# Optimization experiments

Measured on AMD Instinct MI355X. Metric: run time of the kernel, lower is better.

The kernel has to match this reference:

```python
import jax, jax.numpy as jnp
import numpy as np

B, E, S = 32, 1024, 1024


def setup_inputs() -> dict:
    key = jax.random.key(0)
    k_x, k_w = jax.random.split(key)
    x = jax.random.normal(k_x, (B, E, S), dtype=jnp.float32)
    weight = jax.random.normal(k_w, (1, S), dtype=jnp.float32)
    bias = jnp.zeros((S,), dtype=jnp.float32)
    return {"x": x, "weight": weight, "bias": bias}


def _toeplitz(v):
    # v: (m,) -> M[i, j] = v[j - i] if j >= i else 0  (upper-triangular Toeplitz)
    m = v.shape[0]
    i = jnp.arange(m)[:, None]
    j = jnp.arange(m)[None, :]
    return jnp.where(j >= i, v[(j - i) % m], jnp.zeros((), dtype=v.dtype))


def reference(x, weight, bias):
    b, e, s = x.shape
    W = _toeplitz(weight.reshape(-1))          # (S, S)
    out = x.reshape(b * e, s) @ W + bias       # (B*E, S)
    return out.reshape(b, e, s)
```

## Files before the change

kernel.cpp:

```cpp
#include <hip/hip_runtime.h>
#include <stdint.h>

typedef __bf16 bf16x8 __attribute__((ext_vector_type(8)));
typedef float  f32x4  __attribute__((ext_vector_type(4)));

static constexpr int S_DIM = 1024;

__device__ __forceinline__ ushort f32_to_bf16_rne(float f) {
    uint32_t u = __builtin_bit_cast(uint32_t, f);
    u += 0x7fffu + ((u >> 16) & 1u);
    return (ushort)(u >> 16);
}
__device__ __forceinline__ uint32_t pk_bf16(float a, float b) {
    return (uint32_t)f32_to_bf16_rne(a) | ((uint32_t)f32_to_bf16_rne(b) << 16);
}

__global__ void build_wc(const float* __restrict__ w, ushort* __restrict__ Wc) {
    int c  = blockIdx.x * 256 + threadIdx.x;
    int kq = c >> 10;
    int j  = c & 1023;
    uint32_t p[4];
#pragma unroll
    for (int h = 0; h < 4; ++h) {
        int d0 = j - (kq * 8 + h * 2);
        int d1 = d0 - 1;
        float v0 = (d0 >= 0) ? w[d0] : 0.0f;
        float v1 = (d1 >= 0) ? w[d1] : 0.0f;
        p[h] = (uint32_t)f32_to_bf16_rne(v0) | ((uint32_t)f32_to_bf16_rne(v1) << 16);
    }
    reinterpret_cast<uint4*>(Wc)[c] = make_uint4(p[0], p[1], p[2], p[3]);
}

__global__ __launch_bounds__(512, 2) void toep_rowpanel64(
    const float* __restrict__ x, const ushort* __restrict__ Wc,
    const float* __restrict__ bias, float* __restrict__ out)
{
    __shared__ __align__(16) ushort As[2][2048];

    const int tid  = threadIdx.x;
    const int lane = tid & 63;
    const int w    = tid >> 6;
    const int l15  = lane & 15;
    const int quad = lane >> 4;
    const int m0   = blockIdx.x * 64;

    const int sm = tid >> 3;
    const int kc = tid & 7;
    const float* gx = x + (size_t)(m0 + sm) * S_DIM + kc * 4;
    const int aw = (kc >> 1) * 512 + sm * 8 + (kc & 1) * 4;

    const ushort* gb = Wc + (size_t)quad * 8192 + w * 256 + l15 * 8;

    const int ar0 = quad * 512 + l15 * 8;

    f32x4 acc[4][2][4] = {};

    f32x4 av0 = __builtin_nontemporal_load(reinterpret_cast<const f32x4*>(gx));
    f32x4 av1 = __builtin_nontemporal_load(reinterpret_cast<const f32x4*>(gx + 32));

    for (int it = 0; it < 32; ++it) {
        const int p = it & 1;

        uint32_t c0 = pk_bf16(av0[0], av0[1]);
        uint32_t c1 = pk_bf16(av0[2], av0[3]);
        *reinterpret_cast<uint2*>(&As[p][aw]) = make_uint2(c0, c1);

        bool g[4];
#pragma unroll
        for (int pi = 0; pi < 4; ++pi) g[pi] = (pi * 8 + w) >= it;

        const ushort* gbit = gb + (size_t)it * 32768;
        bf16x8 bf[4][2];
        if (g[0]) {
            bf[0][0] = *reinterpret_cast<const bf16x8*>(gbit + 0 * 2048);
            bf[0][1] = *reinterpret_cast<const bf16x8*>(gbit + 0 * 2048 + 128);
        }
        if (g[1]) {
            bf[1][0] = *reinterpret_cast<const bf16x8*>(gbit + 1 * 2048);
            bf[1][1] = *reinterpret_cast<const bf16x8*>(gbit + 1 * 2048 + 128);
        }
        if (g[2]) {
            bf[2][0] = *reinterpret_cast<const bf16x8*>(gbit + 2 * 2048);
            bf[2][1] = *reinterpret_cast<const bf16x8*>(gbit + 2 * 2048 + 128);
        }
        if (g[3]) {
            bf[3][0] = *reinterpret_cast<const bf16x8*>(gbit + 3 * 2048);
            bf[3][1] = *reinterpret_cast<const bf16x8*>(gbit + 3 * 2048 + 128);
        }

        int itn = it + 2; if (itn > 31) itn = 31;
        f32x4 avn = __builtin_nontemporal_load(reinterpret_cast<const f32x4*>(gx + itn * 32));

        asm volatile("s_waitcnt lgkmcnt(0)" ::: "memory");
        __builtin_amdgcn_s_barrier();
        asm volatile("" ::: "memory");

        bf16x8 af[4];
#pragma unroll
        for (int im = 0; im < 4; ++im)
            af[im] = *reinterpret_cast<const bf16x8*>(&As[p][ar0 + im * 128]);

        if (g[0]) {
#pragma unroll
            for (int h = 0; h < 2; ++h)
#pragma unroll
                for (int im = 0; im < 4; ++im)
                    acc[0][h][im] = __builtin_amdgcn_mfma_f32_16x16x32_bf16(af[im], bf[0][h], acc[0][h][im], 0, 0, 0);
        }
        if (g[1]) {
#pragma unroll
            for (int h = 0; h < 2; ++h)
#pragma unroll
                for (int im = 0; im < 4; ++im)
                    acc[1][h][im] = __builtin_amdgcn_mfma_f32_16x16x32_bf16(af[im], bf[1][h], acc[1][h][im], 0, 0, 0);
        }
        if (g[2]) {
#pragma unroll
            for (int h = 0; h < 2; ++h)
#pragma unroll
                for (int im = 0; im < 4; ++im)
                    acc[2][h][im] = __builtin_amdgcn_mfma_f32_16x16x32_bf16(af[im], bf[2][h], acc[2][h][im], 0, 0, 0);
        }
        if (g[3]) {
#pragma unroll
            for (int h = 0; h < 2; ++h)
#pragma unroll
                for (int im = 0; im < 4; ++im)
                    acc[3][h][im] = __builtin_amdgcn_mfma_f32_16x16x32_bf16(af[im], bf[3][h], acc[3][h][im], 0, 0, 0);
        }

        av0 = av1; av1 = avn;
    }

#pragma unroll
    for (int pi = 0; pi < 4; ++pi) {
        const int colb = pi * 256 + w * 32 + l15;
        const float bv0 = bias[colb];
        const float bv1 = bias[colb + 16];
#pragma unroll
        for (int im = 0; im < 4; ++im) {
            const int row0 = m0 + im * 16 + quad * 4;
            float* op = out + (size_t)row0 * S_DIM + colb;
#pragma unroll
            for (int r = 0; r < 4; ++r) {
                __builtin_nontemporal_store(acc[pi][0][im][r] + bv0, op + (size_t)r * S_DIM);
                __builtin_nontemporal_store(acc[pi][1][im][r] + bv1, op + (size_t)r * S_DIM + 16);
            }
        }
    }
}

extern "C" void kernel_launch(void* const* d_in, const int* in_sizes, int n_in,
                              void* d_out, int out_size, void* d_ws, size_t ws_size,
                              hipStream_t stream) {
    const float* x      = (const float*)d_in[0];
    const float* weight = (const float*)d_in[1];
    const float* bias   = (const float*)d_in[2];
    float* out          = (float*)d_out;

    ushort* Wc = (ushort*)d_ws;

    build_wc<<<512, 256, 0, stream>>>(weight, Wc);
    toep_rowpanel64<<<512, 512, 0, stream>>>(x, Wc, bias, out);
}
```

Measured before the change: 271.6 us.

## Stage A panel in 8-step phases to cut barriers per K iteration

The main loop is regrouped into 4 phases of 8 K-steps. Each phase stages a 64x256 bf16 slab of x in a double-buffered LDS array and prefetches the next slab's eight global loads at the start of the phase. This replaces a block barrier every K-step with one barrier per phase, and lets warps skip masked-out steps without synchronising. The cost is larger LDS use (64 KB) and more live registers for the prefetched vectors, which may hurt occupancy at 2 blocks per CU.

```diff
diff --git a/kernel.cpp b/kernel.cpp
--- a/kernel.cpp
+++ b/kernel.cpp
@@ -31,11 +31,11 @@
     reinterpret_cast<uint4*>(Wc)[c] = make_uint4(p[0], p[1], p[2], p[3]);
 }
 
-__global__ __launch_bounds__(512, 2) void toep_rowpanel64(
+__global__ __launch_bounds__(512, 2) void toep_phase64(
     const float* __restrict__ x, const ushort* __restrict__ Wc,
     const float* __restrict__ bias, float* __restrict__ out)
 {
-    __shared__ __align__(16) ushort As[2][2048];
+    __shared__ __align__(16) ushort As[2][8][2048];
 
     const int tid  = threadIdx.x;
     const int lane = tid & 63;
@@ -55,81 +55,101 @@
 
     f32x4 acc[4][2][4] = {};
 
-    f32x4 av0 = __builtin_nontemporal_load(reinterpret_cast<const f32x4*>(gx));
-    f32x4 av1 = __builtin_nontemporal_load(reinterpret_cast<const f32x4*>(gx + 32));
+    {
+        f32x4 v0[8];
+#pragma unroll
+        for (int kk = 0; kk < 8; ++kk)
+            v0[kk] = __builtin_nontemporal_load(reinterpret_cast<const f32x4*>(gx + kk * 32));
+#pragma unroll
+        for (int kk = 0; kk < 8; ++kk)
+            *reinterpret_cast<uint2*>(&As[0][kk][aw]) =
+                make_uint2(pk_bf16(v0[kk][0], v0[kk][1]), pk_bf16(v0[kk][2], v0[kk][3]));
+    }
+    __syncthreads();
 
-    for (int it = 0; it < 32; ++it) {
-        const int p = it & 1;
+    for (int p = 0; p < 4; ++p) {
+        const int b = p & 1;
+        f32x4 v[8];
 
-        uint32_t c0 = pk_bf16(av0[0], av0[1]);
-        uint32_t c1 = pk_bf16(av0[2], av0[3]);
-        *reinterpret_cast<uint2*>(&As[p][aw]) = make_uint2(c0, c1);
+#pragma unroll
+        for (int kk = 0; kk < 8; ++kk) {
+            const int it = p * 8 + kk;
+            const bool g0 = (w      ) >= it;
+            const bool g1 = (w +  8 ) >= it;
+            const bool g2 = (w + 16 ) >= it;
+            const bool g3 = (w + 24 ) >= it;
+            if (!g3) continue;
 
-        bool g[4];
+            const ushort* gbit = gb + (size_t)it * 32768;
+            bf16x8 bf[4][2];
+            if (g0) {
+                bf[0][0] = *reinterpret_cast<const bf16x8*>(gbit);
+                bf[0][1] = *reinterpret_cast<const bf16x8*>(gbit + 128);
+            }
+            if (g1) {
+                bf[1][0] = *reinterpret_cast<const bf16x8*>(gbit + 2048);
+                bf[1][1] = *reinterpret_cast<const bf16x8*>(gbit + 2048 + 128);
+            }
+            if (g2) {
+                bf[2][0] = *reinterpret_cast<const bf16x8*>(gbit + 4096);
+                bf[2][1] = *reinterpret_cast<const bf16x8*>(gbit + 4096 + 128);
+            }
+            if (g3) {
+                bf[3][0] = *reinterpret_cast<const bf16x8*>(gbit + 6144);
+                bf[3][1] = *reinterpret_cast<const bf16x8*>(gbit + 6144 + 128);
+            }
+
+            if (kk == 0 && p < 3) {
+                const float* gxn = gx + (p + 1) * 256;
 #pragma unroll
-        for (int pi = 0; pi < 4; ++pi) g[pi] = (pi * 8 + w) >= it;
+                for (int j = 0; j < 8; ++j)
+                    v[j] = __builtin_nontemporal_load(reinterpret_cast<const f32x4*>(gxn + j * 32));
+            }
 
-        const ushort* gbit = gb + (size_t)it * 32768;
-        bf16x8 bf[4][2];
-        if (g[0]) {
-            bf[0][0] = *reinterpret_cast<const bf16x8*>(gbit + 0 * 2048);
-            bf[0][1] = *reinterpret_cast<const bf16x8*>(gbit + 0 * 2048 + 128);
-        }
-        if (g[1]) {
-            bf[1][0] = *reinterpret_cast<const bf16x8*>(gbit + 1 * 2048);
-            bf[1][1] = *reinterpret_cast<const bf16x8*>(gbit + 1 * 2048 + 128);
-        }
-        if (g[2]) {
-            bf[2][0] = *reinterpret_cast<const bf16x8*>(gbit + 2 * 2048);
-            bf[2][1] = *reinterpret_cast<const bf16x8*>(gbit + 2 * 2048 + 128);
-        }
-        if (g[3]) {
-            bf[3][0] = *reinterpret_cast<const bf16x8*>(gbit + 3 * 2048);
-            bf[3][1] = *reinterpret_cast<const bf16x8*>(gbit + 3 * 2048 + 128);
+            bf16x8 af[4];
+#pragma unroll
+            for (int im = 0; im < 4; ++im)
+                af[im] = *reinterpret_cast<const bf16x8*>(&As[b][kk][ar0 + im * 128]);
+
+            if (g0) {
+#pragma unroll
+                for (int h = 0; h < 2; ++h)
+#pragma unroll
+                    for (int im = 0; im < 4; ++im)
+                        acc[0][h][im] = __builtin_amdgcn_mfma_f32_16x16x32_bf16(af[im], bf[0][h], acc[0][h][im], 0, 0, 0);
+            }
+            if (g1) {
+#pragma unroll
+                for (int h = 0; h < 2; ++h)
+#pragma unroll
+                    for (int im = 0; im < 4; ++im)
+                        acc[1][h][im] = __builtin_amdgcn_mfma_f32_16x16x32_bf16(af[im], bf[1][h], acc[1][h][im], 0, 0, 0);
+            }
+            if (g2) {
+#pragma unroll
+                for (int h = 0; h < 2; ++h)
+#pragma unroll
+                    for (int im = 0; im < 4; ++im)
+                        acc[2][h][im] = __builtin_amdgcn_mfma_f32_16x16x32_bf16(af[im], bf[2][h], acc[2][h][im], 0, 0, 0);
+            }
+            if (g3) {
+#pragma unroll
+                for (int h = 0; h < 2; ++h)
+#pragma unroll
+                    for (int im = 0; im < 4; ++im)
+                        acc[3][h][im] = __builtin_amdgcn_mfma_f32_16x16x32_bf16(af[im], bf[3][h], acc[3][h][im], 0, 0, 0);
+            }
         }
 
-        int itn = it + 2; if (itn > 31) itn = 31;
-        f32x4 avn = __builtin_nontemporal_load(reinterpret_cast<const f32x4*>(gx + itn * 32));
-
-        asm volatile("s_waitcnt lgkmcnt(0)" ::: "memory");
-        __builtin_amdgcn_s_barrier();
-        asm volatile("" ::: "memory");
-
-        bf16x8 af[4];
+        if (p < 3) {
 #pragma unroll
-        for (int im = 0; im < 4; ++im)
-            af[im] = *reinterpret_cast<const bf16x8*>(&As[p][ar0 + im * 128]);
-
-        if (g[0]) {
-#pragma unroll
-            for (int h = 0; h < 2; ++h)
-#pragma unroll
-                for (int im = 0; im < 4; ++im)
-                    acc[0][h][im] = __builtin_amdgcn_mfma_f32_16x16x32_bf16(af[im], bf[0][h], acc[0][h][im], 0, 0, 0);
+            for (int kk = 0; kk < 8; ++kk)
+                *reinterpret_cast<uint2*>(&As[b ^ 1][kk][aw]) =
+                    make_uint2(pk_bf16(v[kk][0], v[kk][1]), pk_bf16(v[kk][2], v[kk][3]));
+            asm volatile("s_waitcnt lgkmcnt(0)" ::: "memory");
+            __builtin_amdgcn_s_barrier();
+            asm volatile("" ::: "memory");
         }
-        if (g[1]) {
-#pragma unroll
-            for (int h = 0; h < 2; ++h)
-#pragma unroll
-                for (int im = 0; im < 4; ++im)
-                    acc[1][h][im] = __builtin_amdgcn_mfma_f32_16x16x32_bf16(af[im], bf[1][h], acc[1][h][im], 0, 0, 0);
-        }
-        if (g[2]) {
-#pragma unroll
-            for (int h = 0; h < 2; ++h)
-#pragma unroll
-                for (int im = 0; im < 4; ++im)
-                    acc[2][h][im] = __builtin_amdgcn_mfma_f32_16x16x32_bf16(af[im], bf[2][h], acc[2][h][im], 0, 0, 0);
-        }
-        if (g[3]) {
-#pragma unroll
-            for (int h = 0; h < 2; ++h)
-#pragma unroll
-                for (int im = 0; im < 4; ++im)
-                    acc[3][h][im] = __builtin_amdgcn_mfma_f32_16x16x32_bf16(af[im], bf[3][h], acc[3][h][im], 0, 0, 0);
-        }
-
-        av0 = av1; av1 = avn;
     }
 
 #pragma unroll
@@ -161,5 +181,5 @@
     ushort* Wc = (ushort*)d_ws;
 
     build_wc<<<512, 256, 0, stream>>>(weight, Wc);
-    toep_rowpanel64<<<512, 512, 0, stream>>>(x, Wc, bias, out);
+    toep_phase64<<<512, 512, 0, stream>>>(x, Wc, bias, out);
 }
```

Result: faster. 263.8 us (-2.9%).
